# Performance work log

Hardware: AMD Instinct MI355X
Metric: run time of the kernel (lower is better)

The kernel has to match this reference:

```python
import jax, jax.numpy as jnp
import numpy as np

B, S, D, H = 2, 2048, 1024, 16
HD = D // H  # head_dim = 64
INIT_STD = 0.02


def rotate_half(x):
    half = x.shape[-1] // 2
    return jnp.concatenate((-x[..., half:], x[..., :half]), axis=-1)


def setup_inputs() -> dict:
    key = jax.random.key(0)
    ks = jax.random.split(key, 6)
    inputs_q = jax.random.normal(ks[0], (B, S, D), dtype=jnp.float32)
    # causal mask, shape [B, 1, S, S] (broadcasts over heads)
    mask = jnp.broadcast_to(jnp.tril(jnp.ones((S, S), dtype=bool))[None, None], (B, 1, S, S))
    Wq = jax.random.normal(ks[1], (D, D), dtype=jnp.float32) * INIT_STD
    Wk = jax.random.normal(ks[2], (D, D), dtype=jnp.float32) * INIT_STD
    Wv = jax.random.normal(ks[3], (D, D), dtype=jnp.float32) * INIT_STD
    Wo = jax.random.normal(ks[4], (D, D), dtype=jnp.float32) * INIT_STD
    bq = jnp.zeros((D,), jnp.float32)
    bk = jnp.zeros((D,), jnp.float32)
    bv = jnp.zeros((D,), jnp.float32)
    bo = jnp.zeros((D,), jnp.float32)
    return {"inputs_q": inputs_q, "mask": mask, "Wq": Wq, "bq": bq, "Wk": Wk, "bk": bk,
            "Wv": Wv, "bv": bv, "Wo": Wo, "bo": bo}


def reference(inputs_q, mask, Wq, bq, Wk, bk, Wv, bv, Wo, bo):
    b, s, d = inputs_q.shape
    h, hd = H, d // H
    # QKV projections, split heads -> [b, s, h, hd]
    q = (inputs_q @ Wq + bq).reshape(b, s, h, hd)
    k = (inputs_q @ Wk + bk).reshape(b, s, h, hd)
    v = (inputs_q @ Wv + bv).reshape(b, s, h, hd)
    # rotary position embedding (GPT-J/Llama style: duplicated freqs over halves)
    pos = jnp.arange(s, dtype=jnp.float32)
    inv_freq = 1.0 / (10000.0 ** (jnp.arange(0, hd, 2, dtype=jnp.float32) / hd))
    freqs = pos[:, None] * inv_freq[None, :]              # [s, hd//2]
    emb = jnp.concatenate((freqs, freqs), axis=-1)        # [s, hd]
    sin = jnp.sin(emb)[None, :, None, :]                  # [1, s, 1, hd]
    cos = jnp.cos(emb)[None, :, None, :]
    q = q * cos + rotate_half(q) * sin
    k = k * cos + rotate_half(k) * sin
    # additive attention bias from boolean mask
    bias = jnp.where(mask, 0.0, jnp.finfo(jnp.float32).min)  # [b, 1, s, s]
    scores = jnp.einsum('bqhd,bkhd->bhqk', q, k) / jnp.sqrt(jnp.float32(hd)) + bias
    attn = jax.nn.softmax(scores, axis=-1)                   # [b, h, q, k]
    out = jnp.einsum('bhqk,bkhd->bqhd', attn, v).reshape(b, s, d)
    return out @ Wo + bo
```

## Files before the change

kernel.cpp:

```cpp
#include <hip/hip_runtime.h>
#include <math.h>

typedef unsigned short u16;
typedef unsigned int   u32;
typedef __attribute__((ext_vector_type(8))) short bf16x8;
typedef __attribute__((ext_vector_type(4))) short s16x4;
typedef __attribute__((ext_vector_type(4))) float f32x4;

#define BB 2
#define SS 2048
#define DD 1024
#define HH 16
#define HD 64
#define MM (BB*SS)
#define QKVN 3072

__device__ __forceinline__ u16 f2bf(float f) {
    u32 u = __float_as_uint(f);
    return (u16)((u + 0x7fffu + ((u >> 16) & 1u)) >> 16);
}
__device__ __forceinline__ float bf2f(u16 h) {
    return __uint_as_float(((u32)h) << 16);
}
__device__ __forceinline__ u32 cvt_pk_bf16(float lo, float hi) {
    u32 r;
    asm("v_cvt_pk_bf16_f32 %0, %1, %2" : "=v"(r) : "v"(lo), "v"(hi));
    return r;
}
__device__ __forceinline__ void gload16(const void* g, void* l) {
    __builtin_amdgcn_global_load_lds(
        (const __attribute__((address_space(1))) u32*)g,
        (__attribute__((address_space(3))) u32*)l, 16, 0, 0);
}

__global__ __launch_bounds__(256) void cast_f32_bf16(
        const float* __restrict__ src, u16* __restrict__ dst, int n4) {
    int i = blockIdx.x * 256 + threadIdx.x;
    if (i >= n4) return;
    float4 v = reinterpret_cast<const float4*>(src)[i];
    u32 lo = (u32)f2bf(v.x) | ((u32)f2bf(v.y) << 16);
    u32 hi = (u32)f2bf(v.z) | ((u32)f2bf(v.w) << 16);
    reinterpret_cast<uint2*>(dst)[i] = make_uint2(lo, hi);
}

__global__ __launch_bounds__(256) void concat_bias(
        const float* __restrict__ a, const float* __restrict__ b,
        const float* __restrict__ c, float* __restrict__ o) {
    int i = blockIdx.x * 256 + threadIdx.x;
    float v = (i < 1024) ? a[i] : (i < 2048) ? b[i - 1024] : c[i - 2048];
    o[i] = v;
}

__global__ __launch_bounds__(256) void transpose_cast_w(
        const float* __restrict__ W0, const float* __restrict__ W1,
        const float* __restrict__ W2, const float* __restrict__ W3,
        u16* __restrict__ T0, u16* __restrict__ T1,
        u16* __restrict__ T2, u16* __restrict__ T3) {
    const float* W; u16* T;
    switch (blockIdx.z) {
        case 0:  W = W0; T = T0; break;
        case 1:  W = W1; T = T1; break;
        case 2:  W = W2; T = T2; break;
        default: W = W3; T = T3; break;
    }
    __shared__ float L[64][65];
    const int t  = threadIdx.x;
    const int k0 = blockIdx.x * 64, n0 = blockIdx.y * 64;
    #pragma unroll
    for (int rep = 0; rep < 4; ++rep) {
        int row = rep * 16 + (t >> 4);
        int col = (t & 15) * 4;
        float4 v = *reinterpret_cast<const float4*>(&W[(size_t)(k0 + row) * DD + n0 + col]);
        L[row][col] = v.x; L[row][col+1] = v.y; L[row][col+2] = v.z; L[row][col+3] = v.w;
    }
    __syncthreads();
    #pragma unroll
    for (int rep = 0; rep < 2; ++rep) {
        int q  = t + rep * 256;
        int n  = q >> 3, sl = q & 7;
        u32 w[4];
        #pragma unroll
        for (int e = 0; e < 4; ++e) {
            float a = L[sl*8 + 2*e][n];
            float b = L[sl*8 + 2*e + 1][n];
            w[e] = (u32)f2bf(a) | ((u32)f2bf(b) << 16);
        }
        *reinterpret_cast<uint4*>(&T[(size_t)(n0 + n) * DD + k0 + sl*8]) =
            make_uint4(w[0], w[1], w[2], w[3]);
    }
}

template <typename OT, int BN, bool ROPE>
__global__ __launch_bounds__(256) void gemm_bf16(
        const u16* __restrict__ A, const u16* __restrict__ Bt,
        const float* __restrict__ bias, OT* __restrict__ C, int N) {
    constexpr int K = DD;
    constexpr int NJ = BN / 32;
    __shared__ __align__(16) u16 As[2][128 * 32];
    __shared__ __align__(16) u16 Bs[2][BN * 32];
    const int tid  = threadIdx.x;
    const int lane = tid & 63, w = tid >> 6;
    const int g = lane >> 4, c = lane & 15;
    const int wr = w >> 1, wc = w & 1;
    const int rowbase = blockIdx.x * 128;
    const int colbase = blockIdx.y * BN;

    auto stage = [&](int t, int bf) {
        const int k0 = t * 32;
        #pragma unroll
        for (int i = 0; i < 2; ++i) {
            int row = w * 32 + i * 16 + (lane >> 2);
            int sl  = lane & 3;
            gload16(&A [(size_t)(rowbase + row) * K + k0 + sl * 8],
                    &As[bf][(w * 32 + i * 16) * 32]);
        }
        #pragma unroll
        for (int i = 0; i < BN / 64; ++i) {
            int rb  = w * (BN / 4) + i * 16;
            int row = rb + (lane >> 2);
            int sl  = lane & 3;
            gload16(&Bt[(size_t)(colbase + row) * K + k0 + sl * 8],
                    &Bs[bf][rb * 32]);
        }
    };

    f32x4 acc[4][NJ];
    #pragma unroll
    for (int i = 0; i < 4; ++i)
        #pragma unroll
        for (int j = 0; j < NJ; ++j) acc[i][j] = (f32x4){0.f, 0.f, 0.f, 0.f};

    stage(0, 0);
    __syncthreads();

    for (int t = 0; t < K / 32; ++t) {
        const int cur = t & 1;
        if (t + 1 < K / 32) stage(t + 1, cur ^ 1);
        bf16x8 af[4], bfr[NJ];
        #pragma unroll
        for (int mi = 0; mi < 4; ++mi)
            af[mi] = *reinterpret_cast<const bf16x8*>(
                &As[cur][(wr * 64 + mi * 16 + c) * 32 + g * 8]);
        #pragma unroll
        for (int nj = 0; nj < NJ; ++nj)
            bfr[nj] = *reinterpret_cast<const bf16x8*>(
                &Bs[cur][(wc * (BN / 2) + nj * 16 + c) * 32 + g * 8]);
        #pragma unroll
        for (int mi = 0; mi < 4; ++mi)
            #pragma unroll
            for (int nj = 0; nj < NJ; ++nj)
                acc[mi][nj] = __builtin_amdgcn_mfma_f32_16x16x32_bf16(
                    af[mi], bfr[nj], acc[mi][nj], 0, 0, 0);
        __syncthreads();
    }

    if constexpr (ROPE) {
        const int region = colbase >> 10;
        const float invf0 = exp2f(-0.41524101186f * (float)c);
        const float invf1 = exp2f(-0.41524101186f * (float)(16 + c));
        #pragma unroll
        for (int mi = 0; mi < 4; ++mi)
            #pragma unroll
            for (int r = 0; r < 4; ++r) {
                const int rowg = rowbase + wr * 64 + mi * 16 + g * 4 + r;
                const float s = (float)(rowg & (SS - 1));
                #pragma unroll
                for (int nj = 0; nj < 2; ++nj) {
                    const int col_lo = colbase + wc * 64 + nj * 16 + c;
                    float lo = acc[mi][nj][r]     + bias[col_lo];
                    float hi = acc[mi][nj + 2][r] + bias[col_lo + 32];
                    if (region < 2) {
                        const float f = s * (nj ? invf1 : invf0);
                        float sn, cs;
                        __sincosf(f, &sn, &cs);
                        float rlo = lo * cs - hi * sn;
                        float rhi = hi * cs + lo * sn;
                        if (region == 0) { rlo *= 0.125f; rhi *= 0.125f; }
                        lo = rlo; hi = rhi;
                    }
                    C[(size_t)rowg * N + col_lo]      = (OT)f2bf(lo);
                    C[(size_t)rowg * N + col_lo + 32] = (OT)f2bf(hi);
                }
            }
    } else {
        #pragma unroll
        for (int mi = 0; mi < 4; ++mi)
            #pragma unroll
            for (int nj = 0; nj < NJ; ++nj) {
                int colg = colbase + wc * (BN / 2) + nj * 16 + c;
                float bv = bias[colg];
                #pragma unroll
                for (int r = 0; r < 4; ++r) {
                    int rowg = rowbase + wr * 64 + mi * 16 + g * 4 + r;
                    float v = acc[mi][nj][r] + bv;
                    if constexpr (sizeof(OT) == 2) C[(size_t)rowg * N + colg] = (OT)f2bf(v);
                    else                           C[(size_t)rowg * N + colg] = v;
                }
            }
    }
}

__global__ __launch_bounds__(512) void attn_mfma(
        const u16* __restrict__ qb, const u16* __restrict__ kb,
        const u16* __restrict__ vb, u16* __restrict__ ob) {
    const int bid = blockIdx.x;
    const int bh  = bid & 31;
    const int p   = bid >> 5;
    const int b   = bh >> 4, h = bh & 15;
    const int tid = threadIdx.x;
    const int lane = tid & 63, wq = tid >> 6;
    const int g = lane >> 4, c = lane & 15;

    __shared__ u16 Ks[2][64 * 64];
    __shared__ u16 Vt[2][64 * 66];

    uint4 kreg, vreg;
    const int krow = tid >> 3;
    const int ksl  = tid & 7;

    auto load_tile = [&](int kt) {
        const size_t base = (size_t)(b * SS + kt * 64 + krow) * QKVN + h * 64 + ksl * 8;
        kreg = *reinterpret_cast<const uint4*>(&kb[base]);
        vreg = *reinterpret_cast<const uint4*>(&vb[base]);
    };
    auto write_tile = [&](int bf) {
        *reinterpret_cast<uint4*>(&Ks[bf][krow * 64 + ((ksl ^ (krow & 7)) * 8)]) = kreg;
        u32 ww[4] = {vreg.x, vreg.y, vreg.z, vreg.w};
        #pragma unroll
        for (int e = 0; e < 4; ++e) {
            Vt[bf][(ksl * 8 + 2 * e    ) * 66 + krow] = (u16)(ww[e] & 0xffffu);
            Vt[bf][(ksl * 8 + 2 * e + 1) * 66 + krow] = (u16)(ww[e] >> 16);
        }
    };

    for (int half = 0; half < 2; ++half) {
        const int qt  = half ? p : (15 - p);
        const int qw0 = qt * 128 + wq * 16;
        const int nkt = qt * 2 + 2;

        bf16x8 qf[2];
        #pragma unroll
        for (int ks = 0; ks < 2; ++ks)
            qf[ks] = *reinterpret_cast<const bf16x8*>(
                &qb[(size_t)(b * SS + qw0 + c) * QKVN + h*64 + ks*32 + g*8]);

        f32x4 of[4];
        #pragma unroll
        for (int i = 0; i < 4; ++i) of[i] = (f32x4){0.f, 0.f, 0.f, 0.f};
        float mv = -1e30f;
        float lv = 0.f;

        load_tile(0);
        __syncthreads();
        write_tile(0);

        for (int kt = 0; kt < nkt; ++kt) {
            const int cur = kt & 1;
            const int k0  = kt * 64;
            if (kt + 1 < nkt) load_tile(kt + 1);
            __syncthreads();

            if (k0 <= qw0 + 15) {
                f32x4 sf[4];
                #pragma unroll
                for (int i = 0; i < 4; ++i) sf[i] = (f32x4){0.f, 0.f, 0.f, 0.f};
                __builtin_amdgcn_s_setprio(1);
                #pragma unroll
                for (int ks = 0; ks < 2; ++ks)
                    #pragma unroll
                    for (int mi = 0; mi < 4; ++mi) {
                        int row = mi*16 + c;
                        bf16x8 kf = *reinterpret_cast<const bf16x8*>(
                            &Ks[cur][row*64 + (((ks*4 + g) ^ (row & 7)) * 8)]);
                        sf[mi] = __builtin_amdgcn_mfma_f32_16x16x32_bf16(
                            kf, qf[ks], sf[mi], 0, 0, 0);
                    }
                __builtin_amdgcn_s_setprio(0);

                if (k0 + 64 > qw0) {
                    const int qv = qw0 + c;
                    #pragma unroll
                    for (int mi = 0; mi < 4; ++mi) {
                        int key = k0 + mi*16 + g*4;
                        #pragma unroll
                        for (int r = 0; r < 4; ++r)
                            if (key + r > qv) sf[mi][r] = -1e30f;
                    }
                }

                float pmax = -1e30f;
                #pragma unroll
                for (int mi = 0; mi < 4; ++mi)
                    #pragma unroll
                    for (int r = 0; r < 4; ++r) pmax = fmaxf(pmax, sf[mi][r]);
                pmax = fmaxf(pmax, __shfl_xor(pmax, 16));
                pmax = fmaxf(pmax, __shfl_xor(pmax, 32));
                if (!__all(pmax - mv <= 8.0f)) {
                    float mnew = fmaxf(mv, pmax);
                    float corr = __expf(mv - mnew);
                    mv = mnew;
                    lv *= corr;
                    #pragma unroll
                    for (int mid = 0; mid < 4; ++mid) of[mid] *= corr;
                }
                float pp[4][4]; float ls = 0.f;
                #pragma unroll
                for (int mi = 0; mi < 4; ++mi)
                    #pragma unroll
                    for (int r = 0; r < 4; ++r) {
                        float e = __expf(sf[mi][r] - mv);
                        pp[mi][r] = e; ls += e;
                    }
                ls += __shfl_xor(ls, 16);
                ls += __shfl_xor(ls, 32);
                lv += ls;
                union PB { u32 u[4]; bf16x8 v; } pb[2];
                #pragma unroll
                for (int ks = 0; ks < 2; ++ks) {
                    pb[ks].u[0] = cvt_pk_bf16(pp[2*ks][0],     pp[2*ks][1]);
                    pb[ks].u[1] = cvt_pk_bf16(pp[2*ks][2],     pp[2*ks][3]);
                    pb[ks].u[2] = cvt_pk_bf16(pp[2*ks + 1][0], pp[2*ks + 1][1]);
                    pb[ks].u[3] = cvt_pk_bf16(pp[2*ks + 1][2], pp[2*ks + 1][3]);
                }

                __builtin_amdgcn_s_setprio(1);
                #pragma unroll
                for (int mid = 0; mid < 4; ++mid) {
                    int d = mid*16 + c;
                    #pragma unroll
                    for (int ks = 0; ks < 2; ++ks) {
                        union { s16x4 hh[2]; bf16x8 v; } vv;
                        vv.hh[0] = *reinterpret_cast<const s16x4*>(&Vt[cur][d*66 + ks*32 + 4*g]);
                        vv.hh[1] = *reinterpret_cast<const s16x4*>(&Vt[cur][d*66 + ks*32 + 16 + 4*g]);
                        of[mid] = __builtin_amdgcn_mfma_f32_16x16x32_bf16(
                            vv.v, pb[ks].v, of[mid], 0, 0, 0);
                    }
                }
                __builtin_amdgcn_s_setprio(0);
            }

            if (kt + 1 < nkt) write_tile(cur ^ 1);
        }

        {
            float inv = 1.0f / lv;
            int qv = qw0 + c;
            #pragma unroll
            for (int mid = 0; mid < 4; ++mid) {
                u32 lo = cvt_pk_bf16(of[mid][0] * inv, of[mid][1] * inv);
                u32 hi = cvt_pk_bf16(of[mid][2] * inv, of[mid][3] * inv);
                *reinterpret_cast<uint2*>(
                    &ob[(size_t)(b * SS + qv) * DD + h*64 + mid*16 + g*4]) =
                    make_uint2(lo, hi);
            }
        }
    }
}

extern "C" void kernel_launch(void* const* d_in, const int* in_sizes, int n_in,
                              void* d_out, int out_size, void* d_ws, size_t ws_size,
                              hipStream_t stream) {
    const float* x  = (const float*)d_in[0];
    const float* Wq = (const float*)d_in[2];
    const float* bq = (const float*)d_in[3];
    const float* Wk = (const float*)d_in[4];
    const float* bk = (const float*)d_in[5];
    const float* Wv = (const float*)d_in[6];
    const float* bv = (const float*)d_in[7];
    const float* Wo = (const float*)d_in[8];
    const float* bo = (const float*)d_in[9];
    float* out = (float*)d_out;

    u16* Xb   = (u16*)d_ws;
    u16* Wcat = Xb   + (size_t)MM * DD;
    u16* Wot  = Wcat + (size_t)3 * DD * DD;
    u16* qkv  = Wot  + (size_t)DD * DD;
    u16* abuf = qkv  + (size_t)MM * QKVN;
    float* bcat = (float*)(abuf + (size_t)MM * DD);

    cast_f32_bf16<<<(MM * DD / 4) / 256, 256, 0, stream>>>(x, Xb, MM * DD / 4);
    concat_bias<<<12, 256, 0, stream>>>(bq, bk, bv, bcat);
    transpose_cast_w<<<dim3(16, 16, 4), 256, 0, stream>>>(
        Wq, Wk, Wv, Wo,
        Wcat, Wcat + (size_t)DD * DD, Wcat + (size_t)2 * DD * DD, Wot);

    gemm_bf16<u16, 128, true><<<dim3(32, 24), 256, 0, stream>>>(Xb, Wcat, bcat, qkv, QKVN);

    attn_mfma<<<256, 512, 0, stream>>>(qkv, qkv + 1024, qkv + 2048, abuf);

    gemm_bf16<float, 64, false><<<dim3(32, 16), 256, 0, stream>>>(abuf, Wot, bo, out, DD);
}
```

Before: 125.3 us.

## Pre-transpose V into a separate buffer and use exp2-domain softmax

Adds a transpose_v kernel that writes V as [b,h,d,s], so attention can load V tiles with one 16-byte LDS store instead of eight scalar transposed stores per thread. Folds log2(e) into the Q scale so softmax uses exp2f, and loosens the lazy-rescale threshold to match the base-2 domain. Reuses the Xb buffer for the attention output to save workspace. The cost is an extra kernel launch and an extra round trip of V through global memory.

```diff
diff --git a/kernel.cpp b/kernel.cpp
--- a/kernel.cpp
+++ b/kernel.cpp
@@ -86,6 +86,39 @@
             w[e] = (u32)f2bf(a) | ((u32)f2bf(b) << 16);
         }
         *reinterpret_cast<uint4*>(&T[(size_t)(n0 + n) * DD + k0 + sl*8]) =
+            make_uint4(w[0], w[1], w[2], w[3]);
+    }
+}
+
+__global__ __launch_bounds__(256) void transpose_v(
+        const u16* __restrict__ qkv, u16* __restrict__ vt) {
+    __shared__ __align__(16) u16 L[64 * 72];
+    const int t  = threadIdx.x;
+    const int s0 = blockIdx.x * 64;
+    const int h  = blockIdx.y;
+    const int b  = blockIdx.z;
+    #pragma unroll
+    for (int rep = 0; rep < 2; ++rep) {
+        int srow = rep * 32 + (t >> 3);
+        int scol = (t & 7) * 8;
+        uint4 v = *reinterpret_cast<const uint4*>(
+            &qkv[(size_t)(b * SS + s0 + srow) * QKVN + 2048 + h * 64 + scol]);
+        *reinterpret_cast<uint4*>(&L[srow * 72 + scol]) = v;
+    }
+    __syncthreads();
+    #pragma unroll
+    for (int rep = 0; rep < 2; ++rep) {
+        int drow = rep * 32 + (t >> 3);
+        int ssl  = t & 7;
+        u32 w[4];
+        #pragma unroll
+        for (int e = 0; e < 4; ++e) {
+            u32 lo = L[(ssl * 8 + 2 * e    ) * 72 + drow];
+            u32 hi = L[(ssl * 8 + 2 * e + 1) * 72 + drow];
+            w[e] = lo | (hi << 16);
+        }
+        *reinterpret_cast<uint4*>(
+            &vt[((size_t)(b * HH + h) * 64 + drow) * SS + s0 + ssl * 8]) =
             make_uint4(w[0], w[1], w[2], w[3]);
     }
 }
@@ -156,6 +189,7 @@
 
     if constexpr (ROPE) {
         const int region = colbase >> 10;
+        const float QSC = 0.18033688011f;
         const float invf0 = exp2f(-0.41524101186f * (float)c);
         const float invf1 = exp2f(-0.41524101186f * (float)(16 + c));
         #pragma unroll
@@ -175,7 +209,7 @@
                         __sincosf(f, &sn, &cs);
                         float rlo = lo * cs - hi * sn;
                         float rhi = hi * cs + lo * sn;
-                        if (region == 0) { rlo *= 0.125f; rhi *= 0.125f; }
+                        if (region == 0) { rlo *= QSC; rhi *= QSC; }
                         lo = rlo; hi = rhi;
                     }
                     C[(size_t)rowg * N + col_lo]      = (OT)f2bf(lo);
@@ -202,7 +236,7 @@
 
 __global__ __launch_bounds__(512) void attn_mfma(
         const u16* __restrict__ qb, const u16* __restrict__ kb,
-        const u16* __restrict__ vb, u16* __restrict__ ob) {
+        const u16* __restrict__ vt, u16* __restrict__ ob) {
     const int bid = blockIdx.x;
     const int bh  = bid & 31;
     const int p   = bid >> 5;
@@ -212,25 +246,21 @@
     const int g = lane >> 4, c = lane & 15;
 
     __shared__ u16 Ks[2][64 * 64];
-    __shared__ u16 Vt[2][64 * 66];
+    __shared__ __align__(16) u16 Vt[2][64 * 72];
 
     uint4 kreg, vreg;
     const int krow = tid >> 3;
     const int ksl  = tid & 7;
 
     auto load_tile = [&](int kt) {
-        const size_t base = (size_t)(b * SS + kt * 64 + krow) * QKVN + h * 64 + ksl * 8;
-        kreg = *reinterpret_cast<const uint4*>(&kb[base]);
-        vreg = *reinterpret_cast<const uint4*>(&vb[base]);
+        kreg = *reinterpret_cast<const uint4*>(
+            &kb[(size_t)(b * SS + kt * 64 + krow) * QKVN + h * 64 + ksl * 8]);
+        vreg = *reinterpret_cast<const uint4*>(
+            &vt[((size_t)bh * 64 + krow) * SS + kt * 64 + ksl * 8]);
     };
     auto write_tile = [&](int bf) {
         *reinterpret_cast<uint4*>(&Ks[bf][krow * 64 + ((ksl ^ (krow & 7)) * 8)]) = kreg;
-        u32 ww[4] = {vreg.x, vreg.y, vreg.z, vreg.w};
-        #pragma unroll
-        for (int e = 0; e < 4; ++e) {
-            Vt[bf][(ksl * 8 + 2 * e    ) * 66 + krow] = (u16)(ww[e] & 0xffffu);
-            Vt[bf][(ksl * 8 + 2 * e + 1) * 66 + krow] = (u16)(ww[e] >> 16);
-        }
+        *reinterpret_cast<uint4*>(&Vt[bf][krow * 72 + ksl * 8]) = vreg;
     };
 
     for (int half = 0; half < 2; ++half) {
@@ -295,9 +325,9 @@
                     for (int r = 0; r < 4; ++r) pmax = fmaxf(pmax, sf[mi][r]);
                 pmax = fmaxf(pmax, __shfl_xor(pmax, 16));
                 pmax = fmaxf(pmax, __shfl_xor(pmax, 32));
-                if (!__all(pmax - mv <= 8.0f)) {
+                if (!__all(pmax - mv <= 11.5f)) {
                     float mnew = fmaxf(mv, pmax);
-                    float corr = __expf(mv - mnew);
+                    float corr = exp2f(mv - mnew);
                     mv = mnew;
                     lv *= corr;
                     #pragma unroll
@@ -308,7 +338,7 @@
                 for (int mi = 0; mi < 4; ++mi)
                     #pragma unroll
                     for (int r = 0; r < 4; ++r) {
-                        float e = __expf(sf[mi][r] - mv);
+                        float e = exp2f(sf[mi][r] - mv);
                         pp[mi][r] = e; ls += e;
                     }
                 ls += __shfl_xor(ls, 16);
@@ -330,8 +360,8 @@
                     #pragma unroll
                     for (int ks = 0; ks < 2; ++ks) {
                         union { s16x4 hh[2]; bf16x8 v; } vv;
-                        vv.hh[0] = *reinterpret_cast<const s16x4*>(&Vt[cur][d*66 + ks*32 + 4*g]);
-                        vv.hh[1] = *reinterpret_cast<const s16x4*>(&Vt[cur][d*66 + ks*32 + 16 + 4*g]);
+                        vv.hh[0] = *reinterpret_cast<const s16x4*>(&Vt[cur][d*72 + ks*32 + 4*g]);
+                        vv.hh[1] = *reinterpret_cast<const s16x4*>(&Vt[cur][d*72 + ks*32 + 16 + 4*g]);
                         of[mid] = __builtin_amdgcn_mfma_f32_16x16x32_bf16(
                             vv.v, pb[ks].v, of[mid], 0, 0, 0);
                     }
@@ -375,8 +405,9 @@
     u16* Wcat = Xb   + (size_t)MM * DD;
     u16* Wot  = Wcat + (size_t)3 * DD * DD;
     u16* qkv  = Wot  + (size_t)DD * DD;
-    u16* abuf = qkv  + (size_t)MM * QKVN;
-    float* bcat = (float*)(abuf + (size_t)MM * DD);
+    u16* vt   = qkv  + (size_t)MM * QKVN;
+    float* bcat = (float*)(vt + (size_t)BB * HH * 64 * SS);
+    u16* abuf = Xb;
 
     cast_f32_bf16<<<(MM * DD / 4) / 256, 256, 0, stream>>>(x, Xb, MM * DD / 4);
     concat_bias<<<12, 256, 0, stream>>>(bq, bk, bv, bcat);
@@ -386,7 +417,9 @@
 
     gemm_bf16<u16, 128, true><<<dim3(32, 24), 256, 0, stream>>>(Xb, Wcat, bcat, qkv, QKVN);
 
-    attn_mfma<<<256, 512, 0, stream>>>(qkv, qkv + 1024, qkv + 2048, abuf);
+    transpose_v<<<dim3(SS / 64, HH, BB), 256, 0, stream>>>(qkv, vt);
+
+    attn_mfma<<<256, 512, 0, stream>>>(qkv, qkv + 1024, vt, abuf);
 
     gemm_bf16<float, 64, false><<<dim3(32, 16), 256, 0, stream>>>(abuf, Wot, bo, out, DD);
 }
```

Result: slower. 134.4 us (+7.3%).
